# Optimization experiments

Measured on AMD Instinct MI355X. Metric: run time of the kernel, lower is better.

The kernel has to match this reference:

```python
import jax, jax.numpy as jnp
import numpy as np

EPS = 1e-7  # K.epsilon()

def squash(v, axis=-1):
    sn = jnp.sum(jnp.square(v), axis=axis, keepdims=True)
    scale = sn / (1.0 + sn) / jnp.sqrt(sn + EPS)
    return scale * v

def setup_inputs() -> dict:
    key = jax.random.key(0)
    k1, k2, k3 = jax.random.split(key, 3)
    B, In, Din = 32, 2048, 8
    N, Dout, C = 64, 16, 32
    x = jax.random.normal(k1, (B, In, Din), dtype=jnp.float32)
    W = jax.random.normal(k2, (N, C, Dout, Din), dtype=jnp.float32) * 0.1
    B_bias = jax.random.normal(k3, (N, Dout), dtype=jnp.float32) * 0.1
    return {"x": x, "W": W, "B_bias": B_bias}

def reference(x, W, B_bias):
    routings = 3
    N, C, Dout, Din = W.shape
    In = x.shape[1]
    # repeat channel weights to cover all input capsules: [N, In, Dout, Din]
    W2 = jnp.repeat(W, In // C, axis=1)
    # vote vectors: inputs_hat[b,n,i,d] = sum_k x[b,i,k] * W2[n,i,d,k]
    inputs_hat = jnp.einsum('bik,nidk->bnid', x, W2)  # [B, N, In, Dout]
    b = jnp.zeros(inputs_hat.shape[:3], dtype=inputs_hat.dtype)  # [B, N, In]
    outputs = None
    for i in range(routings):
        c = jax.nn.softmax(b, axis=1)  # softmax over num_capsule axis
        s = jnp.einsum('bni,bnid->bnd', c, inputs_hat) + B_bias
        outputs = squash(s)
        if i < routings - 1:
            b = b + jnp.einsum('bnd,bnid->bni', outputs, inputs_hat)
    return outputs
```

## Files before the change

kernel.cpp:

```cpp
#include <hip/hip_runtime.h>
#include <hip/hip_cooperative_groups.h>
#include <math.h>

namespace cg = cooperative_groups;

constexpr int B_    = 32;
constexpr int In_   = 2048;
constexpr int Din_  = 8;
constexpr int N_    = 64;
constexpr int Dout_ = 16;
constexpr int C_    = 32;
constexpr int ICP   = 64;
constexpr int GRID  = 512;
constexpr float EPS = 1e-7f;

struct Smem {
    float Us[N_][8];
    float xs[ICP][8];
    float lg[ICP][68];
    float ps[4][ICP];
    float inv_s[ICP];
    float ys[4][N_][8];
};

__device__ __forceinline__ void v0_body(
    Smem* sm, int blk,
    const float* __restrict__ x, const float* __restrict__ W,
    const float* __restrict__ bias, float* __restrict__ v0)
{
    const int b = blk >> 3, j = blk & 7;
    const int t = threadIdx.x;
    float (*xbar)[8] = (float(*)[8])(&sm->Us[0][0]);

    {
        const int c = t >> 3, k = t & 7;
        const float* xp = x + (size_t)b * In_ * Din_ + (size_t)c * ICP * Din_ + k;
        float acc = 0.f;
        #pragma unroll 8
        for (int i = 0; i < ICP; ++i) acc += xp[i * Din_];
        xbar[c][k] = acc * (1.f / 64.f);
    }
    __syncthreads();

    {
        const int nl = t >> 5, lane32 = t & 31;
        const int d = lane32 >> 1, h = lane32 & 1;
        const int n = j * 8 + nl;

        float a = 0.f;
        #pragma unroll
        for (int cc = 0; cc < 16; ++cc) {
            const int c2 = cc * 2 + h;
            const float4* wp = (const float4*)(W + (((size_t)n * C_ + c2) * Dout_ + d) * Din_);
            const float4 w0 = wp[0], w1 = wp[1];
            a += w0.x * xbar[c2][0] + w0.y * xbar[c2][1] + w0.z * xbar[c2][2] + w0.w * xbar[c2][3]
               + w1.x * xbar[c2][4] + w1.y * xbar[c2][5] + w1.z * xbar[c2][6] + w1.w * xbar[c2][7];
        }
        a += __shfl_xor(a, 1);
        a += bias[n * Dout_ + d];

        float sn = a * a;
        sn += __shfl_xor(sn, 2);
        sn += __shfl_xor(sn, 4);
        sn += __shfl_xor(sn, 8);
        sn += __shfl_xor(sn, 16);
        const float sc = sn / (1.f + sn) / sqrtf(sn + EPS);
        if (h == 0) v0[(size_t)b * 1024 + n * Dout_ + d] = a * sc;
    }
}

__device__ __forceinline__ void route_body(
    Smem* sm, int blk,
    const float* __restrict__ x, const float* __restrict__ W,
    const float* __restrict__ v_src, float* __restrict__ s_out)
{
    const int b = blk >> 5;
    const int c = blk & 31;
    const int t = threadIdx.x;
    const int w = t >> 6, l = t & 63;
    const int n4 = t >> 2, q4 = t & 3;

    {
        const float4 vv = *(const float4*)(v_src + ((size_t)b * 64 + n4) * 16 + q4 * 4);
        const float vd[4] = {vv.x, vv.y, vv.z, vv.w};
        float pU[8] = {0, 0, 0, 0, 0, 0, 0, 0};
        #pragma unroll
        for (int dd = 0; dd < 4; ++dd) {
            const int d = q4 * 4 + dd;
            const float4* wp = (const float4*)(W + (((size_t)n4 * 32 + c) * 16 + d) * 8);
            const float4 w0 = wp[0], w1 = wp[1];
            const float v_ = vd[dd];
            pU[0] += v_ * w0.x; pU[1] += v_ * w0.y; pU[2] += v_ * w0.z; pU[3] += v_ * w0.w;
            pU[4] += v_ * w1.x; pU[5] += v_ * w1.y; pU[6] += v_ * w1.z; pU[7] += v_ * w1.w;
        }
        #pragma unroll
        for (int k = 0; k < 8; ++k) {
            pU[k] += __shfl_xor(pU[k], 1);
            pU[k] += __shfl_xor(pU[k], 2);
        }
        float2 u2; u2.x = pU[2 * q4]; u2.y = pU[2 * q4 + 1];
        *(float2*)&sm->Us[n4][2 * q4] = u2;
    }

    float xr[8];
    {
        const float4* xp = (const float4*)(x + ((size_t)b * In_ + c * ICP + l) * 8);
        const float4 x0 = xp[0], x1 = xp[1];
        xr[0] = x0.x; xr[1] = x0.y; xr[2] = x0.z; xr[3] = x0.w;
        xr[4] = x1.x; xr[5] = x1.y; xr[6] = x1.z; xr[7] = x1.w;
        if (w == 0) { *(float4*)&sm->xs[l][0] = x0; *(float4*)&sm->xs[l][4] = x1; }
    }
    __syncthreads();

    {
        float e[16];
        float ssum = 0.f;
        #pragma unroll
        for (int nn = 0; nn < 16; ++nn) {
            const int n = w * 16 + nn;
            const float4 u0 = *(const float4*)&sm->Us[n][0];
            const float4 u1 = *(const float4*)&sm->Us[n][4];
            const float a = u0.x * xr[0] + u0.y * xr[1] + u0.z * xr[2] + u0.w * xr[3]
                          + u1.x * xr[4] + u1.y * xr[5] + u1.z * xr[6] + u1.w * xr[7];
            const float ee = __expf(a);
            e[nn] = ee; ssum += ee;
        }
        #pragma unroll
        for (int qq = 0; qq < 4; ++qq) {
            float4 o;
            o.x = e[qq * 4 + 0]; o.y = e[qq * 4 + 1]; o.z = e[qq * 4 + 2]; o.w = e[qq * 4 + 3];
            *(float4*)&sm->lg[l][w * 16 + qq * 4] = o;
        }
        sm->ps[w][l] = ssum;
    }
    __syncthreads();

    if (t < 64) sm->inv_s[t] = 1.f / (sm->ps[0][t] + sm->ps[1][t] + sm->ps[2][t] + sm->ps[3][t]);
    __syncthreads();

    {
        const int nq = l >> 2, kq = l & 3;
        float y[8] = {0, 0, 0, 0, 0, 0, 0, 0};
        #pragma unroll
        for (int ii = 0; ii < 16; ++ii) {
            const int i = w * 16 + ii;
            const float4 cw = *(const float4*)&sm->lg[i][nq * 4];
            const float iv = sm->inv_s[i];
            const float2 x2 = *(const float2*)&sm->xs[i][kq * 2];
            const float c0 = cw.x * iv, c1 = cw.y * iv, c2 = cw.z * iv, c3 = cw.w * iv;
            y[0] += c0 * x2.x; y[1] += c0 * x2.y;
            y[2] += c1 * x2.x; y[3] += c1 * x2.y;
            y[4] += c2 * x2.x; y[5] += c2 * x2.y;
            y[6] += c3 * x2.x; y[7] += c3 * x2.y;
        }
        #pragma unroll
        for (int jj = 0; jj < 4; ++jj) {
            float2 o; o.x = y[2 * jj]; o.y = y[2 * jj + 1];
            *(float2*)&sm->ys[w][nq * 4 + jj][kq * 2] = o;
        }
    }
    __syncthreads();

    {
        float yn[8];
        #pragma unroll
        for (int k = 0; k < 8; ++k)
            yn[k] = sm->ys[0][n4][k] + sm->ys[1][n4][k] + sm->ys[2][n4][k] + sm->ys[3][n4][k];
        float4 o;
        float* op = (float*)&o;
        #pragma unroll
        for (int dd = 0; dd < 4; ++dd) {
            const int d = q4 * 4 + dd;
            const float4* wp = (const float4*)(W + (((size_t)n4 * 32 + c) * 16 + d) * 8);
            const float4 w0 = wp[0], w1 = wp[1];
            op[dd] = w0.x * yn[0] + w0.y * yn[1] + w0.z * yn[2] + w0.w * yn[3]
                   + w1.x * yn[4] + w1.y * yn[5] + w1.z * yn[6] + w1.w * yn[7];
        }
        *(float4*)(s_out + (((size_t)b * 32 + c) * 64 + n4) * 16 + q4 * 4) = o;
    }
}

__device__ __forceinline__ void reduce_body(
    int blk, const float* __restrict__ s_src, const float* __restrict__ bias,
    const float* __restrict__ vadd, float* __restrict__ dst)
{
    const int b = blk >> 3, j = blk & 7;
    const int t = threadIdx.x;
    const int nl = t >> 5, lane32 = t & 31;
    const int d = lane32 >> 1, h = lane32 & 1;
    const int n = j * 8 + nl;

    float a = 0.f;
    #pragma unroll
    for (int cc = 0; cc < 16; ++cc) {
        const int c2 = cc * 2 + h;
        a += s_src[(((size_t)b * 32 + c2) * 64 + n) * 16 + d];
    }
    a += __shfl_xor(a, 1);
    a += bias[n * Dout_ + d];

    float sn = a * a;
    sn += __shfl_xor(sn, 2);
    sn += __shfl_xor(sn, 4);
    sn += __shfl_xor(sn, 8);
    sn += __shfl_xor(sn, 16);
    const float sc = sn / (1.f + sn) / sqrtf(sn + EPS);
    float val = a * sc;
    if (vadd) val += vadd[(size_t)b * 1024 + n * Dout_ + d];
    if (h == 0) dst[(size_t)b * 1024 + n * Dout_ + d] = val;
}

__global__ __launch_bounds__(256, 2) void caps_fused(
    const float* __restrict__ x, const float* __restrict__ W,
    const float* __restrict__ bias, float* __restrict__ out,
    float* __restrict__ s1, float* __restrict__ s2,
    float* __restrict__ v0, float* __restrict__ vsum)
{
    __shared__ Smem sm;
    cg::grid_group grid = cg::this_grid();
    const int blk = blockIdx.x;

    if (blk < 256) v0_body(&sm, blk, x, W, bias, v0);
    grid.sync();

    route_body(&sm, blk, x, W, v0, s1);
    __syncthreads();
    route_body(&sm, blk + 512, x, W, v0, s1);
    grid.sync();

    if (blk < 256) reduce_body(blk, s1, bias, v0, vsum);
    grid.sync();

    route_body(&sm, blk, x, W, vsum, s2);
    __syncthreads();
    route_body(&sm, blk + 512, x, W, vsum, s2);
    grid.sync();

    if (blk < 256) reduce_body(blk, s2, bias, nullptr, out);
}

__global__ __launch_bounds__(256) void caps_v0_k(
    const float* __restrict__ x, const float* __restrict__ W,
    const float* __restrict__ bias, float* __restrict__ v0)
{
    __shared__ Smem sm;
    v0_body(&sm, blockIdx.x, x, W, bias, v0);
}

__global__ __launch_bounds__(256) void caps_route_k(
    const float* __restrict__ x, const float* __restrict__ W,
    const float* __restrict__ v_src, float* __restrict__ s_out)
{
    __shared__ Smem sm;
    route_body(&sm, blockIdx.x, x, W, v_src, s_out);
}

__global__ __launch_bounds__(256) void caps_reduce_k(
    const float* __restrict__ s_src, const float* __restrict__ bias,
    const float* __restrict__ vadd, float* __restrict__ dst)
{
    reduce_body(blockIdx.x, s_src, bias, vadd, dst);
}

extern "C" void kernel_launch(void* const* d_in, const int* in_sizes, int n_in,
                              void* d_out, int out_size, void* d_ws, size_t ws_size,
                              hipStream_t stream) {
    const float* x    = (const float*)d_in[0];
    const float* W    = (const float*)d_in[1];
    const float* bias = (const float*)d_in[2];
    float* out = (float*)d_out;

    float* ws   = (float*)d_ws;
    float* s1   = ws;
    float* s2   = s1   + (size_t)B_ * C_ * N_ * Dout_;
    float* v0   = s2   + (size_t)B_ * C_ * N_ * Dout_;
    float* vsum = v0   + (size_t)B_ * N_ * Dout_;

    static int use_coop = -1;
    if (use_coop < 0) {
        int dev = 0;
        (void)hipGetDevice(&dev);
        int occ = 0;
        (void)hipOccupancyMaxActiveBlocksPerMultiprocessor(
            &occ, (const void*)caps_fused, 256, 0);
        int cus = 0;
        (void)hipDeviceGetAttribute(&cus, hipDeviceAttributeMultiprocessorCount, dev);
        use_coop = (occ > 0 && cus > 0 && (long)occ * (long)cus >= GRID) ? 1 : 0;
    }

    if (use_coop) {
        void* args[] = {
            (void*)&x, (void*)&W, (void*)&bias, (void*)&out,
            (void*)&s1, (void*)&s2, (void*)&v0, (void*)&vsum
        };
        hipError_t e = hipLaunchCooperativeKernel((void*)caps_fused, dim3(GRID),
                                                  dim3(256), args, 0, stream);
        if (e == hipSuccess) return;
        use_coop = 0;
    }

    caps_v0_k    <<<256,  256, 0, stream>>>(x, W, bias, v0);
    caps_route_k <<<1024, 256, 0, stream>>>(x, W, v0, s1);
    caps_reduce_k<<<256,  256, 0, stream>>>(s1, bias, v0, vsum);
    caps_route_k <<<1024, 256, 0, stream>>>(x, W, vsum, s2);
    caps_reduce_k<<<256,  256, 0, stream>>>(s2, bias, nullptr, out);
}
```

Before: 92.55 us.

## Replace cooperative grid sync with custom atomic barriers and fold vsum reduction

```diff
diff --git a/kernel.cpp b/kernel.cpp
--- a/kernel.cpp
+++ b/kernel.cpp
@@ -1,8 +1,5 @@
 #include <hip/hip_runtime.h>
-#include <hip/hip_cooperative_groups.h>
 #include <math.h>
-
-namespace cg = cooperative_groups;
 
 constexpr int B_    = 32;
 constexpr int In_   = 2048;
@@ -23,6 +20,25 @@
     float ys[4][N_][8];
 };
 
+__device__ __forceinline__ void gbar(unsigned* cnt, unsigned* flag, unsigned nb)
+{
+    __syncthreads();
+    if (threadIdx.x == 0) {
+        __threadfence();
+        const unsigned old = __hip_atomic_fetch_add(
+            cnt, 1u, __ATOMIC_ACQ_REL, __HIP_MEMORY_SCOPE_AGENT);
+        if (old == nb - 1u) {
+            __hip_atomic_store(flag, 1u, __ATOMIC_RELEASE, __HIP_MEMORY_SCOPE_AGENT);
+        } else {
+            while (__hip_atomic_load(flag, __ATOMIC_ACQUIRE,
+                                     __HIP_MEMORY_SCOPE_AGENT) == 0u)
+                __builtin_amdgcn_s_sleep(8);
+        }
+        __threadfence();
+    }
+    __syncthreads();
+}
+
 __device__ __forceinline__ void v0_body(
     Smem* sm, int blk,
     const float* __restrict__ x, const float* __restrict__ W,
@@ -70,18 +86,15 @@
 }
 
 __device__ __forceinline__ void route_body(
-    Smem* sm, int blk,
+    Smem* sm, int b, int c, float4 vv,
     const float* __restrict__ x, const float* __restrict__ W,
-    const float* __restrict__ v_src, float* __restrict__ s_out)
-{
-    const int b = blk >> 5;
-    const int c = blk & 31;
+    float* __restrict__ s_out)
+{
     const int t = threadIdx.x;
     const int w = t >> 6, l = t & 63;
     const int n4 = t >> 2, q4 = t & 3;
 
     {
-        const float4 vv = *(const float4*)(v_src + ((size_t)b * 64 + n4) * 16 + q4 * 4);
         const float vd[4] = {vv.x, vv.y, vv.z, vv.w};
         float pU[8] = {0, 0, 0, 0, 0, 0, 0, 0};
         #pragma unroll
@@ -180,9 +193,36 @@
     }
 }
 
+__device__ __forceinline__ float4 vsum_tile(
+    int b, const float* __restrict__ s1, const float* __restrict__ bias,
+    const float* __restrict__ v0buf)
+{
+    const int t = threadIdx.x, n4 = t >> 2, q4 = t & 3;
+    float a0 = 0.f, a1 = 0.f, a2 = 0.f, a3 = 0.f;
+    const float* sp = s1 + ((size_t)b * 32 * 64 + n4) * 16 + q4 * 4;
+    #pragma unroll 8
+    for (int c = 0; c < 32; ++c) {
+        const float4 sv = *(const float4*)(sp + (size_t)c * 1024);
+        a0 += sv.x; a1 += sv.y; a2 += sv.z; a3 += sv.w;
+    }
+    const float4 bi = *(const float4*)(bias + n4 * 16 + q4 * 4);
+    a0 += bi.x; a1 += bi.y; a2 += bi.z; a3 += bi.w;
+
+    float sn = a0 * a0 + a1 * a1 + a2 * a2 + a3 * a3;
+    sn += __shfl_xor(sn, 1);
+    sn += __shfl_xor(sn, 2);
+    const float sc = sn / (1.f + sn) / sqrtf(sn + EPS);
+
+    const float4 v0v = *(const float4*)(v0buf + (size_t)b * 1024 + n4 * 16 + q4 * 4);
+    float4 r;
+    r.x = v0v.x + a0 * sc; r.y = v0v.y + a1 * sc;
+    r.z = v0v.z + a2 * sc; r.w = v0v.w + a3 * sc;
+    return r;
+}
+
 __device__ __forceinline__ void reduce_body(
     int blk, const float* __restrict__ s_src, const float* __restrict__ bias,
-    const float* __restrict__ vadd, float* __restrict__ dst)
+    float* __restrict__ dst)
 {
     const int b = blk >> 3, j = blk & 7;
     const int t = threadIdx.x;
@@ -205,61 +245,47 @@
     sn += __shfl_xor(sn, 8);
     sn += __shfl_xor(sn, 16);
     const float sc = sn / (1.f + sn) / sqrtf(sn + EPS);
-    float val = a * sc;
-    if (vadd) val += vadd[(size_t)b * 1024 + n * Dout_ + d];
-    if (h == 0) dst[(size_t)b * 1024 + n * Dout_ + d] = val;
-}
-
-__global__ __launch_bounds__(256, 2) void caps_fused(
+    if (h == 0) dst[(size_t)b * 1024 + n * Dout_ + d] = a * sc;
+}
+
+__global__ __launch_bounds__(256, 2) void caps_persist(
     const float* __restrict__ x, const float* __restrict__ W,
     const float* __restrict__ bias, float* __restrict__ out,
     float* __restrict__ s1, float* __restrict__ s2,
-    float* __restrict__ v0, float* __restrict__ vsum)
+    float* __restrict__ v0buf, unsigned* __restrict__ bar)
 {
     __shared__ Smem sm;
-    cg::grid_group grid = cg::this_grid();
     const int blk = blockIdx.x;
-
-    if (blk < 256) v0_body(&sm, blk, x, W, bias, v0);
-    grid.sync();
-
-    route_body(&sm, blk, x, W, v0, s1);
-    __syncthreads();
-    route_body(&sm, blk + 512, x, W, v0, s1);
-    grid.sync();
-
-    if (blk < 256) reduce_body(blk, s1, bias, v0, vsum);
-    grid.sync();
-
-    route_body(&sm, blk, x, W, vsum, s2);
-    __syncthreads();
-    route_body(&sm, blk + 512, x, W, vsum, s2);
-    grid.sync();
-
-    if (blk < 256) reduce_body(blk, s2, bias, nullptr, out);
-}
-
-__global__ __launch_bounds__(256) void caps_v0_k(
-    const float* __restrict__ x, const float* __restrict__ W,
-    const float* __restrict__ bias, float* __restrict__ v0)
-{
-    __shared__ Smem sm;
-    v0_body(&sm, blockIdx.x, x, W, bias, v0);
-}
-
-__global__ __launch_bounds__(256) void caps_route_k(
-    const float* __restrict__ x, const float* __restrict__ W,
-    const float* __restrict__ v_src, float* __restrict__ s_out)
-{
-    __shared__ Smem sm;
-    route_body(&sm, blockIdx.x, x, W, v_src, s_out);
-}
-
-__global__ __launch_bounds__(256) void caps_reduce_k(
-    const float* __restrict__ s_src, const float* __restrict__ bias,
-    const float* __restrict__ vadd, float* __restrict__ dst)
-{
-    reduce_body(blockIdx.x, s_src, bias, vadd, dst);
+    const int n4 = threadIdx.x >> 2, q4 = threadIdx.x & 3;
+
+    if (blk < 256) v0_body(&sm, blk, x, W, bias, v0buf);
+    gbar(&bar[0], &bar[1], GRID);
+
+    {
+        int b = blk >> 5, c = blk & 31;
+        float4 vv = *(const float4*)(v0buf + ((size_t)b * 64 + n4) * 16 + q4 * 4);
+        route_body(&sm, b, c, vv, x, W, s1);
+        __syncthreads();
+        const int blk2 = blk + GRID;
+        b = blk2 >> 5; c = blk2 & 31;
+        vv = *(const float4*)(v0buf + ((size_t)b * 64 + n4) * 16 + q4 * 4);
+        route_body(&sm, b, c, vv, x, W, s1);
+    }
+    gbar(&bar[32], &bar[33], GRID);
+
+    {
+        int b = blk >> 5, c = blk & 31;
+        float4 vv = vsum_tile(b, s1, bias, v0buf);
+        route_body(&sm, b, c, vv, x, W, s2);
+        __syncthreads();
+        const int blk2 = blk + GRID;
+        b = blk2 >> 5; c = blk2 & 31;
+        vv = vsum_tile(b, s1, bias, v0buf);
+        route_body(&sm, b, c, vv, x, W, s2);
+    }
+    gbar(&bar[64], &bar[65], GRID);
+
+    if (blk < 256) reduce_body(blk, s2, bias, out);
 }
 
 extern "C" void kernel_launch(void* const* d_in, const int* in_sizes, int n_in,
@@ -272,36 +298,11 @@
 
     float* ws   = (float*)d_ws;
     float* s1   = ws;
-    float* s2   = s1   + (size_t)B_ * C_ * N_ * Dout_;
-    float* v0   = s2   + (size_t)B_ * C_ * N_ * Dout_;
-    float* vsum = v0   + (size_t)B_ * N_ * Dout_;
-
-    static int use_coop = -1;
-    if (use_coop < 0) {
-        int dev = 0;
-        (void)hipGetDevice(&dev);
-        int occ = 0;
-        (void)hipOccupancyMaxActiveBlocksPerMultiprocessor(
-            &occ, (const void*)caps_fused, 256, 0);
-        int cus = 0;
-        (void)hipDeviceGetAttribute(&cus, hipDeviceAttributeMultiprocessorCount, dev);
-        use_coop = (occ > 0 && cus > 0 && (long)occ * (long)cus >= GRID) ? 1 : 0;
-    }
-
-    if (use_coop) {
-        void* args[] = {
-            (void*)&x, (void*)&W, (void*)&bias, (void*)&out,
-            (void*)&s1, (void*)&s2, (void*)&v0, (void*)&vsum
-        };
-        hipError_t e = hipLaunchCooperativeKernel((void*)caps_fused, dim3(GRID),
-                                                  dim3(256), args, 0, stream);
-        if (e == hipSuccess) return;
-        use_coop = 0;
-    }
-
-    caps_v0_k    <<<256,  256, 0, stream>>>(x, W, bias, v0);
-    caps_route_k <<<1024, 256, 0, stream>>>(x, W, v0, s1);
-    caps_reduce_k<<<256,  256, 0, stream>>>(s1, bias, v0, vsum);
-    caps_route_k <<<1024, 256, 0, stream>>>(x, W, vsum, s2);
-    caps_reduce_k<<<256,  256, 0, stream>>>(s2, bias, nullptr, out);
-}
+    float* s2   = s1 + (size_t)B_ * C_ * N_ * Dout_;
+    float* v0b  = s2 + (size_t)B_ * C_ * N_ * Dout_;
+    unsigned* bar = (unsigned*)(v0b + (size_t)B_ * N_ * Dout_);
+
+    hipMemsetAsync(bar, 0, 96 * sizeof(unsigned), stream);
+
+    caps_persist<<<GRID, 256, 0, stream>>>(x, W, bias, out, s1, s2, v0b, bar);
+}
```

After: 306.6 us. +231.3%, slower.
